# Optimization experiments

Measured on AMD Instinct MI355X. Metric: run time of the kernel, lower is better.

Reference implementation:

```python
import jax, jax.numpy as jnp
import numpy as np

N = 8192          # tokens
CD = 512          # coarse_dim
FD = 512          # fine_dim
CB = 4096         # coarse codebook size
FB = 8192         # fine codebook size
COST = 0.25       # commitment cost
LRELU = 0.1
EPS = 1e-5


def _vq(x, emb):
    # squared-distance cdist: [n, K]
    d = jnp.sum(x * x, axis=1, keepdims=True) + jnp.sum(emb * emb, axis=1) - 2.0 * (x @ emb.T)
    idx = jnp.argmin(d, axis=1)          # temperature=1.0 (updates=0); scaling doesn't change argmin
    q = emb[idx]                          # gather == one-hot @ emb, without materializing one-hot
    e_loss = jnp.mean((jax.lax.stop_gradient(q) - x) ** 2)
    q_loss = jnp.mean((q - jax.lax.stop_gradient(x)) ** 2)
    loss = q_loss + COST * e_loss
    q_st = x + jax.lax.stop_gradient(q - x)   # straight-through
    return q_st, loss


def _mlp(x, w, b, g, be):
    # Linear (torch: x @ W.T + b) -> LayerNorm -> LeakyReLU(0.1)
    h = x @ w.T + b
    m = jnp.mean(h, axis=-1, keepdims=True)
    v = jnp.var(h, axis=-1, keepdims=True)
    h = (h - m) / jnp.sqrt(v + EPS) * g + be
    return jnp.where(h > 0, h, LRELU * h)


def setup_inputs() -> dict:
    key = jax.random.key(0)
    ks = jax.random.split(key, 6)
    xav_c = float(np.sqrt(6.0 / (CB + CD)))
    xav_f = float(np.sqrt(6.0 / (FB + FD)))
    lin_s = float(np.sqrt(1.0 / CD))
    return {
        'z': jax.random.normal(ks[0], (N, CD + FD), dtype=jnp.float32),
        'coarse_emb': jax.random.uniform(ks[1], (CB, CD), jnp.float32, -xav_c, xav_c),
        'fine_emb': jax.random.uniform(ks[2], (FB, FD), jnp.float32, -xav_f, xav_f),
        'w_c2f': jax.random.uniform(ks[3], (FD, CD), jnp.float32, -lin_s, lin_s),
        'b_c2f': jnp.zeros((FD,), jnp.float32),
        'g_c2f': jnp.ones((FD,), jnp.float32),
        'be_c2f': jnp.zeros((FD,), jnp.float32),
        'w_f2c': jax.random.uniform(ks[4], (CD, FD), jnp.float32, -lin_s, lin_s),
        'b_f2c': jnp.zeros((CD,), jnp.float32),
        'g_f2c': jnp.ones((CD,), jnp.float32),
        'be_f2c': jnp.zeros((CD,), jnp.float32),
        'gate_c_raw': jnp.float32(0.5),
        'gate_f_raw': jnp.float32(0.5),
    }


def reference(z, coarse_emb, fine_emb, w_c2f, b_c2f, g_c2f, be_c2f,
              w_f2c, b_f2c, g_f2c, be_f2c, gate_c_raw, gate_f_raw):
    split = z.shape[1] // 2
    z_coarse, z_fine = z[:, :split], z[:, split:]

    z_coarse_q, coarse_loss = _vq(z_coarse, coarse_emb)
    coarse_influence = _mlp(jax.lax.stop_gradient(z_coarse_q), w_c2f, b_c2f, g_c2f, be_c2f)
    gate_c = jax.nn.sigmoid(gate_c_raw)

    residual = z_fine - gate_c * coarse_influence
    z_fine_q, fine_loss = _vq(residual, fine_emb)

    fine_feedback = _mlp(jax.lax.stop_gradient(z_fine_q), w_f2c, b_f2c, g_f2c, be_f2c)
    gate_f = jax.nn.sigmoid(gate_f_raw)

    z_coarse_corrected = z_coarse_q + 0.1 * gate_f * fine_feedback
    z_fine_reconstructed = z_fine_q + gate_c * coarse_influence
    z_hierarchical = jnp.concatenate([z_coarse_corrected, z_fine_reconstructed], axis=1)
    vq_loss = coarse_loss + fine_loss
    return z_hierarchical, vq_loss
```

## Files before the change

kernel.cpp:

```cpp
#include <hip/hip_runtime.h>
#include <hip/hip_bf16.h>
#include <cstdint>
#include <cstddef>

#define KD 512

#define OFF_CN   0u
#define OFF_FN   16384u
#define OFF_ZN   49152u
#define OFF_RN   81920u
#define OFF_LOSS 114688u
#define OFF_AMC  114944u
#define OFF_AMF  180480u
#define OFF_CEH  246016u
#define OFF_CEL  4440320u
#define OFF_FEH  8634624u
#define OFF_FEL  17023232u
#define OFF_ZCH  25411840u
#define OFF_ZCL  33800448u
#define OFF_RH   42189056u
#define OFF_RL   50577664u
#define OFF_W1H  58966272u
#define OFF_W1L  59490560u
#define OFF_W2H  60014848u
#define OFF_W2L  60539136u
#define OFF_H    61063424u
#define OFF_INFL 77840640u


typedef __attribute__((ext_vector_type(8))) short bf16x8;
typedef __attribute__((ext_vector_type(4))) float f32x4;

__device__ __forceinline__ bf16x8 as_bf16x8(int4 v) {
  union { int4 i; bf16x8 b; } u; u.i = v; return u.b;
}

__device__ __forceinline__ float block_sum(float v, float* sred) {
#pragma unroll
  for (int off = 32; off > 0; off >>= 1) v += __shfl_down(v, off, 64);
  if ((threadIdx.x & 63) == 0) sred[threadIdx.x >> 6] = v;
  __syncthreads();
  float r = sred[0] + sred[1] + sred[2] + sred[3];
  __syncthreads();
  return r;
}

__device__ __forceinline__ float sigmoidf_(float x) { return 1.0f / (1.0f + expf(-x)); }

__device__ __forceinline__ void split_bf16(float v, __hip_bfloat16* hi, __hip_bfloat16* lo) {
  __hip_bfloat16 h = __float2bfloat16(v);
  *hi = h;
  *lo = __float2bfloat16(v - __bfloat162float(h));
}

__global__ __launch_bounds__(256) void prep(
    const float* __restrict__ ce, const float* __restrict__ fe, const float* __restrict__ z,
    const float* __restrict__ w1, const float* __restrict__ w2,
    float* __restrict__ cn, float* __restrict__ fn, float* __restrict__ zn,
    __hip_bfloat16* __restrict__ ceH, __hip_bfloat16* __restrict__ ceL,
    __hip_bfloat16* __restrict__ feH, __hip_bfloat16* __restrict__ feL,
    __hip_bfloat16* __restrict__ zcH, __hip_bfloat16* __restrict__ zcL,
    __hip_bfloat16* __restrict__ w1H, __hip_bfloat16* __restrict__ w1L,
    __hip_bfloat16* __restrict__ w2H, __hip_bfloat16* __restrict__ w2L,
    float* __restrict__ lossp) {
  __shared__ float sred[4];
  const int b = blockIdx.x, t = threadIdx.x;
  const float* src;
  float* nd = nullptr;
  __hip_bfloat16 *dh, *dl;
  int fragMode = 0;
  size_t row;
  if (b < 4096) {
    row = b; src = ce + row * KD; nd = cn + row; dh = ceH; dl = ceL; fragMode = 1;
  } else if (b < 12288) {
    row = b - 4096; src = fe + row * KD; nd = fn + row; dh = feH; dl = feL; fragMode = 1;
  } else if (b < 20480) {
    row = b - 12288; src = z + row * 1024; nd = zn + row; dh = zcH; dl = zcL;
  } else if (b < 20992) {
    row = b - 20480; src = w1 + row * KD; dh = w1H; dl = w1L;
  } else {
    row = b - 20992; src = w2 + row * KD; dh = w2H; dl = w2L;
  }
  float acc = 0.0f;
  if (fragMode) {
    float v0 = src[t], v1 = src[t + 256];
    acc = v0 * v0 + v1 * v1;
  } else {
#pragma unroll
    for (int j = 0; j < 2; ++j) {
      int c = t + j * 256;
      float v = src[c];
      acc += v * v;
      __hip_bfloat16 h, l;
      split_bf16(v, &h, &l);
      dh[row * KD + c] = h;
      dl[row * KD + c] = l;
    }
  }
  if (nd) {
    float s = block_sum(acc, sred);
    if (t == 0) nd[0] = s;
  } else {
    __syncthreads();
    __syncthreads();
  }
  if (fragMode && t < 64) {
    union { int4 i; __hip_bfloat16 s[8]; } ph, pl;
#pragma unroll
    for (int j = 0; j < 8; ++j) {
      float v = src[8 * t + j];
      split_bf16(v, &ph.s[j], &pl.s[j]);
    }
    const int chunkIdx = (int)(((row >> 4) * 16 + (t >> 2)) * 64 +
                               ((size_t)((t & 3) << 4) | (row & 15)));
    ((int4*)dh)[chunkIdx] = ph.i;
    ((int4*)dl)[chunkIdx] = pl.i;
  }
  if (b == 20480 && t == 0) lossp[0] = 0.0f;
}

__global__ __launch_bounds__(256) void vq6(
    const int4* __restrict__ AfH, const int4* __restrict__ AfL,
    const __hip_bfloat16* __restrict__ Bh, const __hip_bfloat16* __restrict__ Bl,
    const float* __restrict__ qn, const float* __restrict__ cn,
    unsigned long long* __restrict__ amin) {
  __shared__ __align__(16) __hip_bfloat16 sBh[2][128 * 32];
  __shared__ __align__(16) __hip_bfloat16 sBl[2][128 * 32];
  const int t = threadIdx.x;
  const int w = t >> 6, l = t & 63;
  const int rowTile = blockIdx.y << 7;
  const int colTile = blockIdx.x << 7;
  const int wr = (w >> 1) << 6;
  const int wc = (w & 1) << 6;

  const int srow = t >> 2;
  const int sb = t & 3;
  const int skE = sb << 3;
  const int swz = (sb ^ ((srow >> 1) & 3)) << 3;
  const int wOff0 = (srow << 5) + swz;
  const int wOff1 = ((srow + 64) << 5) + swz;
  const size_t br0 = (size_t)(colTile + srow) * KD;
  const size_t br1 = (size_t)(colTile + 64 + srow) * KD;

  const int fr = l & 15;
  const int q = l >> 4;

  int aB[4];
#pragma unroll
  for (int mt = 0; mt < 4; ++mt)
    aB[mt] = (((rowTile + wr + (mt << 4)) >> 4) << 10) + l;

  f32x4 acc[4][4];
#pragma unroll
  for (int i = 0; i < 4; ++i)
#pragma unroll
    for (int j = 0; j < 4; ++j) acc[i][j] = (f32x4){0.f, 0.f, 0.f, 0.f};

  int4 rBh0 = *(const int4*)(Bh + br0 + skE);
  int4 rBh1 = *(const int4*)(Bh + br1 + skE);
  int4 rBl0 = *(const int4*)(Bl + br0 + skE);
  int4 rBl1 = *(const int4*)(Bl + br1 + skE);
  int4 aH[4], aL[4];
#pragma unroll
  for (int mt = 0; mt < 4; ++mt) {
    aH[mt] = AfH[aB[mt]];
    aL[mt] = AfL[aB[mt]];
  }

  int p = 0;
  for (int kk = 0; kk < KD; kk += 32) {
    *(int4*)(sBh[p] + wOff0) = rBh0; *(int4*)(sBh[p] + wOff1) = rBh1;
    *(int4*)(sBl[p] + wOff0) = rBl0; *(int4*)(sBl[p] + wOff1) = rBl1;
    __syncthreads();

    bf16x8 afh[4], afl[4];
#pragma unroll
    for (int mt = 0; mt < 4; ++mt) {
      afh[mt] = as_bf16x8(aH[mt]);
      afl[mt] = as_bf16x8(aL[mt]);
    }

    const int nkc = (kk + 32 < KD) ? ((kk >> 5) + 1) : 0;
    const int nkE = nkc << 5;
    rBh0 = *(const int4*)(Bh + br0 + nkE + skE);
    rBh1 = *(const int4*)(Bh + br1 + nkE + skE);
    rBl0 = *(const int4*)(Bl + br0 + nkE + skE);
    rBl1 = *(const int4*)(Bl + br1 + nkE + skE);
#pragma unroll
    for (int mt = 0; mt < 4; ++mt) {
      aH[mt] = AfH[aB[mt] + (nkc << 6)];
      aL[mt] = AfL[aB[mt] + (nkc << 6)];
    }

    bf16x8 bfh[4], bfl[4];
#pragma unroll
    for (int nt = 0; nt < 4; ++nt) {
      const int rB = wc + (nt << 4) + fr;
      const int o = (rB << 5) + ((q ^ ((rB >> 1) & 3)) << 3);
      bfh[nt] = *(const bf16x8*)(sBh[p] + o);
      bfl[nt] = *(const bf16x8*)(sBl[p] + o);
    }
#pragma unroll
    for (int mt = 0; mt < 4; ++mt)
#pragma unroll
      for (int nt = 0; nt < 4; ++nt) {
        acc[mt][nt] = __builtin_amdgcn_mfma_f32_16x16x32_bf16(afh[mt], bfh[nt], acc[mt][nt], 0, 0, 0);
        acc[mt][nt] = __builtin_amdgcn_mfma_f32_16x16x32_bf16(afh[mt], bfl[nt], acc[mt][nt], 0, 0, 0);
        acc[mt][nt] = __builtin_amdgcn_mfma_f32_16x16x32_bf16(afl[mt], bfh[nt], acc[mt][nt], 0, 0, 0);
      }
    p ^= 1;
  }

#pragma unroll
  for (int nt = 0; nt < 4; ++nt) {
    const int query = colTile + wc + (nt << 4) + fr;
    const float xn = qn[query];
    unsigned long long key = ~0ULL;
#pragma unroll
    for (int mt = 0; mt < 4; ++mt) {
#pragma unroll
      for (int reg = 0; reg < 4; ++reg) {
        const int code = rowTile + wr + (mt << 4) + (q << 2) + reg;
        float d = (xn + cn[code]) - 2.0f * acc[mt][nt][reg];
        unsigned ub = __float_as_uint(d);
        ub = (ub & 0x80000000u) ? ~ub : (ub | 0x80000000u);
        unsigned long long k2 = ((unsigned long long)ub << 32) | (unsigned long long)(unsigned)code;
        if (k2 < key) key = k2;
      }
    }
    unsigned long long o1 = __shfl_xor(key, 16, 64);
    if (o1 < key) key = o1;
    unsigned long long o2 = __shfl_xor(key, 32, 64);
    if (o2 < key) key = o2;
    if (l < 16) atomicMin(amin + colTile + wc + (nt << 4) + l, key);
  }
}

__global__ __launch_bounds__(256) void mlp6(
    const int4* __restrict__ AfH, const int4* __restrict__ AfL,
    const unsigned long long* __restrict__ gather,
    const __hip_bfloat16* __restrict__ Bh, const __hip_bfloat16* __restrict__ Bl,
    const float* __restrict__ bias, float* __restrict__ C) {
  __shared__ __align__(16) __hip_bfloat16 sAh[128 * 32];
  __shared__ __align__(16) __hip_bfloat16 sAl[128 * 32];
  __shared__ __align__(16) __hip_bfloat16 sBh[128 * 32];
  __shared__ __align__(16) __hip_bfloat16 sBl[128 * 32];
  const int t = threadIdx.x;
  const int w = t >> 6, l = t & 63;
  const int rowTile = blockIdx.y << 7;
  const int colTile = blockIdx.x << 7;
  const int wr = (w >> 1) << 6;
  const int wc = (w & 1) << 6;

  const int srow = t >> 2;
  const int sb = t & 3;
  const int skE = sb << 3;
  const int swz = (sb ^ ((srow >> 1) & 3)) << 3;
  const int wOff0 = (srow << 5) + swz;
  const int wOff1 = ((srow + 64) << 5) + swz;

  unsigned i0 = ((const unsigned*)gather)[2 * (rowTile + srow)];
  unsigned i1 = ((const unsigned*)gather)[2 * (rowTile + 64 + srow)];
  const int a0 = (int)((i0 >> 4) << 10) + (sb << 4) + (int)(i0 & 15);
  const int a1 = (int)((i1 >> 4) << 10) + (sb << 4) + (int)(i1 & 15);
  const size_t br0 = (size_t)(colTile + srow) * KD;
  const size_t br1 = (size_t)(colTile + 64 + srow) * KD;

  const int fr = l & 15;
  const int q = l >> 4;
  const int foff = (q ^ ((fr >> 1) & 3)) << 3;

  f32x4 acc[4][4];
#pragma unroll
  for (int i = 0; i < 4; ++i)
#pragma unroll
    for (int j = 0; j < 4; ++j) acc[i][j] = (f32x4){0.f, 0.f, 0.f, 0.f};

  for (int kk = 0; kk < KD; kk += 32) {
    const int kc64 = (kk >> 5) << 6;
    int4 vAh0 = AfH[a0 + kc64];
    int4 vAh1 = AfH[a1 + kc64];
    int4 vAl0 = AfL[a0 + kc64];
    int4 vAl1 = AfL[a1 + kc64];
    int4 vBh0 = *(const int4*)(Bh + br0 + kk + skE);
    int4 vBh1 = *(const int4*)(Bh + br1 + kk + skE);
    int4 vBl0 = *(const int4*)(Bl + br0 + kk + skE);
    int4 vBl1 = *(const int4*)(Bl + br1 + kk + skE);
    __syncthreads();
    *(int4*)(sAh + wOff0) = vAh0; *(int4*)(sAh + wOff1) = vAh1;
    *(int4*)(sAl + wOff0) = vAl0; *(int4*)(sAl + wOff1) = vAl1;
    *(int4*)(sBh + wOff0) = vBh0; *(int4*)(sBh + wOff1) = vBh1;
    *(int4*)(sBl + wOff0) = vBl0; *(int4*)(sBl + wOff1) = vBl1;
    __syncthreads();

    bf16x8 afh[4], afl[4], bfh[4], bfl[4];
#pragma unroll
    for (int mt = 0; mt < 4; ++mt) {
      const int rA = wr + (mt << 4) + fr;
      const int o = (rA << 5) + ((q ^ ((rA >> 1) & 3)) << 3);
      afh[mt] = *(const bf16x8*)(sAh + o);
      afl[mt] = *(const bf16x8*)(sAl + o);
    }
#pragma unroll
    for (int nt = 0; nt < 4; ++nt) {
      const int rB = wc + (nt << 4) + fr;
      const int o = (rB << 5) + ((q ^ ((rB >> 1) & 3)) << 3);
      bfh[nt] = *(const bf16x8*)(sBh + o);
      bfl[nt] = *(const bf16x8*)(sBl + o);
    }
#pragma unroll
    for (int mt = 0; mt < 4; ++mt)
#pragma unroll
      for (int nt = 0; nt < 4; ++nt) {
        acc[mt][nt] = __builtin_amdgcn_mfma_f32_16x16x32_bf16(afh[mt], bfh[nt], acc[mt][nt], 0, 0, 0);
        acc[mt][nt] = __builtin_amdgcn_mfma_f32_16x16x32_bf16(afh[mt], bfl[nt], acc[mt][nt], 0, 0, 0);
        acc[mt][nt] = __builtin_amdgcn_mfma_f32_16x16x32_bf16(afl[mt], bfh[nt], acc[mt][nt], 0, 0, 0);
      }
  }

  const int quad = l >> 4;
#pragma unroll
  for (int mt = 0; mt < 4; ++mt) {
#pragma unroll
    for (int reg = 0; reg < 4; ++reg) {
      const int row = rowTile + wr + (mt << 4) + (quad << 2) + reg;
#pragma unroll
      for (int nt = 0; nt < 4; ++nt) {
        const int col = colTile + wc + (nt << 4) + fr;
        C[(size_t)row * KD + col] = acc[mt][nt][reg] + bias[col];
      }
    }
  }
}

__global__ __launch_bounds__(256) void ln_residual(
    const float* __restrict__ h, const float* __restrict__ g, const float* __restrict__ be,
    const float* __restrict__ z, const float* __restrict__ gRaw,
    __hip_bfloat16* __restrict__ infl, float* __restrict__ rn,
    __hip_bfloat16* __restrict__ rH, __hip_bfloat16* __restrict__ rL) {
  __shared__ float sred[4];
  const int row = blockIdx.x, t = threadIdx.x;
  const size_t base = (size_t)row * KD;
  float h0 = h[base + t], h1 = h[base + t + 256];
  float m = block_sum(h0 + h1, sred) * (1.0f / 512.0f);
  float d0 = h0 - m, d1 = h1 - m;
  float var = block_sum(d0 * d0 + d1 * d1, sred) * (1.0f / 512.0f);
  float sq = sqrtf(var + 1e-5f);
  float gc = sigmoidf_(gRaw[0]);
  float v0 = d0 / sq * g[t] + be[t];
  float v1 = d1 / sq * g[t + 256] + be[t + 256];
  v0 = v0 > 0.0f ? v0 : 0.1f * v0;
  v1 = v1 > 0.0f ? v1 : 0.1f * v1;
  infl[base + t] = __float2bfloat16(v0);
  infl[base + t + 256] = __float2bfloat16(v1);
  float zf0 = z[(size_t)row * 1024 + 512 + t];
  float zf1 = z[(size_t)row * 1024 + 512 + t + 256];
  float r0 = zf0 - gc * v0, r1 = zf1 - gc * v1;
  __hip_bfloat16 hh, ll;
  split_bf16(r0, &hh, &ll);
  rH[base + t] = hh; rL[base + t] = ll;
  split_bf16(r1, &hh, &ll);
  rH[base + t + 256] = hh; rL[base + t + 256] = ll;
  float rs = block_sum(r0 * r0 + r1 * r1, sred);
  if (t == 0) rn[row] = rs;
}

__global__ __launch_bounds__(256) void finalize(
    const float* __restrict__ h, const float* __restrict__ g, const float* __restrict__ be,
    const __hip_bfloat16* __restrict__ infl,
    const unsigned long long* __restrict__ amc, const unsigned long long* __restrict__ amf,
    const float* __restrict__ z, const float* __restrict__ ce, const float* __restrict__ fe,
    const float* __restrict__ gcRaw, const float* __restrict__ gfRaw,
    float* __restrict__ out, float* __restrict__ lossp) {
  __shared__ float sred[4];
  const int row = blockIdx.x, t = threadIdx.x;
  const size_t base = (size_t)row * KD;
  float h0 = h[base + t], h1 = h[base + t + 256];
  float m = block_sum(h0 + h1, sred) * (1.0f / 512.0f);
  float d0 = h0 - m, d1 = h1 - m;
  float var = block_sum(d0 * d0 + d1 * d1, sred) * (1.0f / 512.0f);
  float sq = sqrtf(var + 1e-5f);
  float fb0 = d0 / sq * g[t] + be[t];
  float fb1 = d1 / sq * g[t + 256] + be[t + 256];
  fb0 = fb0 > 0.0f ? fb0 : 0.1f * fb0;
  fb1 = fb1 > 0.0f ? fb1 : 0.1f * fb1;
  float gc = sigmoidf_(gcRaw[0]);
  float gf = sigmoidf_(gfRaw[0]);
  unsigned ic = (unsigned)(amc[row] & 0xffffffffULL);
  unsigned ifx = (unsigned)(amf[row] & 0xffffffffULL);
  float loc = 0.0f;
#pragma unroll
  for (int j = 0; j < 2; ++j) {
    int c = t + j * 256;
    float fb = j ? fb1 : fb0;
    float qc = ce[(size_t)ic * KD + c];
    float qf = fe[(size_t)ifx * KD + c];
    float zc = z[(size_t)row * 1024 + c];
    float zf = z[(size_t)row * 1024 + 512 + c];
    float fl = __bfloat162float(infl[base + c]);
    out[(size_t)row * 1024 + c] = qc + 0.1f * gf * fb;
    out[(size_t)row * 1024 + 512 + c] = qf + gc * fl;
    float dc = qc - zc;
    float res = zf - gc * fl;
    float df = qf - res;
    loc += dc * dc + df * df;
  }
  float ls = block_sum(loc, sred);
  if (t == 0) atomicAdd(lossp, ls);
}

__global__ void loss_write(const float* __restrict__ lossp, float* __restrict__ out) {
  out[0] = 1.25f * lossp[0] / (8192.0f * 512.0f);
}

extern "C" void kernel_launch(void* const* d_in, const int* in_sizes, int n_in,
                              void* d_out, int out_size, void* d_ws, size_t ws_size,
                              hipStream_t stream) {
  const float* z      = (const float*)d_in[0];
  const float* ce     = (const float*)d_in[1];
  const float* fe     = (const float*)d_in[2];
  const float* w_c2f  = (const float*)d_in[3];
  const float* b_c2f  = (const float*)d_in[4];
  const float* g_c2f  = (const float*)d_in[5];
  const float* be_c2f = (const float*)d_in[6];
  const float* w_f2c  = (const float*)d_in[7];
  const float* b_f2c  = (const float*)d_in[8];
  const float* g_f2c  = (const float*)d_in[9];
  const float* be_f2c = (const float*)d_in[10];
  const float* gcRaw  = (const float*)d_in[11];
  const float* gfRaw  = (const float*)d_in[12];
  float* out = (float*)d_out;
  char* ws = (char*)d_ws;

  float* cn = (float*)(ws + OFF_CN);
  float* fn = (float*)(ws + OFF_FN);
  float* zn = (float*)(ws + OFF_ZN);
  float* rn = (float*)(ws + OFF_RN);
  float* lossp = (float*)(ws + OFF_LOSS);
  unsigned long long* amc = (unsigned long long*)(ws + OFF_AMC);
  unsigned long long* amf = (unsigned long long*)(ws + OFF_AMF);
  __hip_bfloat16* ceH = (__hip_bfloat16*)(ws + OFF_CEH);
  __hip_bfloat16* ceL = (__hip_bfloat16*)(ws + OFF_CEL);
  __hip_bfloat16* feH = (__hip_bfloat16*)(ws + OFF_FEH);
  __hip_bfloat16* feL = (__hip_bfloat16*)(ws + OFF_FEL);
  __hip_bfloat16* zcH = (__hip_bfloat16*)(ws + OFF_ZCH);
  __hip_bfloat16* zcL = (__hip_bfloat16*)(ws + OFF_ZCL);
  __hip_bfloat16* rH  = (__hip_bfloat16*)(ws + OFF_RH);
  __hip_bfloat16* rL  = (__hip_bfloat16*)(ws + OFF_RL);
  __hip_bfloat16* w1H = (__hip_bfloat16*)(ws + OFF_W1H);
  __hip_bfloat16* w1L = (__hip_bfloat16*)(ws + OFF_W1L);
  __hip_bfloat16* w2H = (__hip_bfloat16*)(ws + OFF_W2H);
  __hip_bfloat16* w2L = (__hip_bfloat16*)(ws + OFF_W2L);
  float* h = (float*)(ws + OFF_H);
  __hip_bfloat16* infl = (__hip_bfloat16*)(ws + OFF_INFL);

  hipMemsetAsync(ws + OFF_AMC, 0xFF, 131072, stream);

  prep<<<21504, 256, 0, stream>>>(ce, fe, z, w_c2f, w_f2c, cn, fn, zn,
                                  ceH, ceL, feH, feL, zcH, zcL,
                                  w1H, w1L, w2H, w2L, lossp);

  vq6<<<dim3(64, 32), 256, 0, stream>>>((const int4*)ceH, (const int4*)ceL,
                                        zcH, zcL, zn, cn, amc);

  mlp6<<<dim3(4, 64), 256, 0, stream>>>((const int4*)ceH, (const int4*)ceL, amc,
                                        w1H, w1L, b_c2f, h);

  ln_residual<<<8192, 256, 0, stream>>>(h, g_c2f, be_c2f, z, gcRaw, infl, rn, rH, rL);

  vq6<<<dim3(64, 64), 256, 0, stream>>>((const int4*)feH, (const int4*)feL,
                                        rH, rL, rn, fn, amf);

  mlp6<<<dim3(4, 64), 256, 0, stream>>>((const int4*)feH, (const int4*)feL, amf,
                                        w2H, w2L, b_f2c, h);

  finalize<<<8192, 256, 0, stream>>>(h, g_f2c, be_f2c, infl, amc, amf, z, ce, fe,
                                     gcRaw, gfRaw, out, lossp);
  loss_write<<<1, 1, 0, stream>>>(lossp, out + (size_t)8192 * 1024);
}
```

Baseline: 640.8 us.

## Stage VQ codebook tiles via direct global-to-LDS loads with triple buffering

The VQ distance GEMM kernel now copies B tiles straight from global memory into LDS with global_load_lds, instead of going through registers and explicit LDS stores. It uses a three-deep LDS ring with prefetch two steps ahead, one barrier per k-step, and a fully unrolled k loop. The XOR swizzle moves from the LDS write address to the global source address. The aim is to free VGPRs and LDS-store issue slots and to hide load latency better, with s_setprio raised around the MFMA block. The cost is more LDS use and reliance on implicit vmcnt waits to order the DMA writes before the reads.

Measured after the change: 622.3 us. 2.9% less time.

```diff
diff --git a/kernel.cpp b/kernel.cpp
--- a/kernel.cpp
+++ b/kernel.cpp
@@ -33,6 +33,12 @@
 
 __device__ __forceinline__ bf16x8 as_bf16x8(int4 v) {
   union { int4 i; bf16x8 b; } u; u.i = v; return u.b;
+}
+
+__device__ __forceinline__ void gl_lds16(const void* g, void* l) {
+  __builtin_amdgcn_global_load_lds(
+      (const __attribute__((address_space(1))) void*)g,
+      (__attribute__((address_space(3))) void*)l, 16, 0, 0);
 }
 
 __device__ __forceinline__ float block_sum(float v, float* sred) {
@@ -119,13 +125,13 @@
   if (b == 20480 && t == 0) lossp[0] = 0.0f;
 }
 
-__global__ __launch_bounds__(256) void vq6(
+__global__ __launch_bounds__(256) void vq7(
     const int4* __restrict__ AfH, const int4* __restrict__ AfL,
     const __hip_bfloat16* __restrict__ Bh, const __hip_bfloat16* __restrict__ Bl,
     const float* __restrict__ qn, const float* __restrict__ cn,
     unsigned long long* __restrict__ amin) {
-  __shared__ __align__(16) __hip_bfloat16 sBh[2][128 * 32];
-  __shared__ __align__(16) __hip_bfloat16 sBl[2][128 * 32];
+  __shared__ __align__(16) __hip_bfloat16 sBh[3][128 * 32];
+  __shared__ __align__(16) __hip_bfloat16 sBl[3][128 * 32];
   const int t = threadIdx.x;
   const int w = t >> 6, l = t & 63;
   const int rowTile = blockIdx.y << 7;
@@ -133,14 +139,12 @@
   const int wr = (w >> 1) << 6;
   const int wc = (w & 1) << 6;
 
-  const int srow = t >> 2;
-  const int sb = t & 3;
-  const int skE = sb << 3;
-  const int swz = (sb ^ ((srow >> 1) & 3)) << 3;
-  const int wOff0 = (srow << 5) + swz;
-  const int wOff1 = ((srow + 64) << 5) + swz;
-  const size_t br0 = (size_t)(colTile + srow) * KD;
-  const size_t br1 = (size_t)(colTile + 64 + srow) * KD;
+  const int rl = l >> 2;
+  const int sbp = (l & 3) ^ ((l >> 3) & 3);
+  const size_t gOff0 = (size_t)(colTile + (w << 5) + rl) * KD + (sbp << 3);
+  const size_t gOff1 = gOff0 + (size_t)16 * KD;
+  const int lOff0 = (w << 5) << 5;
+  const int lOff1 = lOff0 + (16 << 5);
 
   const int fr = l & 15;
   const int q = l >> 4;
@@ -156,22 +160,27 @@
 #pragma unroll
     for (int j = 0; j < 4; ++j) acc[i][j] = (f32x4){0.f, 0.f, 0.f, 0.f};
 
-  int4 rBh0 = *(const int4*)(Bh + br0 + skE);
-  int4 rBh1 = *(const int4*)(Bh + br1 + skE);
-  int4 rBl0 = *(const int4*)(Bl + br0 + skE);
-  int4 rBl1 = *(const int4*)(Bl + br1 + skE);
+#define STAGE_B(bi, ck) do {                                      \
+    gl_lds16(Bh + gOff0 + ((size_t)(ck) << 5), &sBh[bi][lOff0]);  \
+    gl_lds16(Bh + gOff1 + ((size_t)(ck) << 5), &sBh[bi][lOff1]);  \
+    gl_lds16(Bl + gOff0 + ((size_t)(ck) << 5), &sBl[bi][lOff0]);  \
+    gl_lds16(Bl + gOff1 + ((size_t)(ck) << 5), &sBl[bi][lOff1]);  \
+  } while (0)
+
   int4 aH[4], aL[4];
-#pragma unroll
-  for (int mt = 0; mt < 4; ++mt) {
-    aH[mt] = AfH[aB[mt]];
-    aL[mt] = AfL[aB[mt]];
-  }
-
-  int p = 0;
-  for (int kk = 0; kk < KD; kk += 32) {
-    *(int4*)(sBh[p] + wOff0) = rBh0; *(int4*)(sBh[p] + wOff1) = rBh1;
-    *(int4*)(sBl[p] + wOff0) = rBl0; *(int4*)(sBl[p] + wOff1) = rBl1;
-    __syncthreads();
+  STAGE_B(0, 0);
+  STAGE_B(1, 1);
+#pragma unroll
+  for (int mt = 0; mt < 4; ++mt) { aH[mt] = AfH[aB[mt]]; aL[mt] = AfL[aB[mt]]; }
+  __builtin_amdgcn_sched_barrier(0);
+  asm volatile("s_waitcnt vmcnt(0)" ::: "memory");
+
+#pragma unroll
+  for (int i = 0; i < 16; ++i) {
+    __builtin_amdgcn_s_barrier();
+    __builtin_amdgcn_sched_barrier(0);
+    if (i + 2 < 16) STAGE_B((i + 2) % 3, i + 2);
+    __builtin_amdgcn_sched_barrier(0);
 
     bf16x8 afh[4], afl[4];
 #pragma unroll
@@ -179,26 +188,24 @@
       afh[mt] = as_bf16x8(aH[mt]);
       afl[mt] = as_bf16x8(aL[mt]);
     }
-
-    const int nkc = (kk + 32 < KD) ? ((kk >> 5) + 1) : 0;
-    const int nkE = nkc << 5;
-    rBh0 = *(const int4*)(Bh + br0 + nkE + skE);
-    rBh1 = *(const int4*)(Bh + br1 + nkE + skE);
-    rBl0 = *(const int4*)(Bl + br0 + nkE + skE);
-    rBl1 = *(const int4*)(Bl + br1 + nkE + skE);
-#pragma unroll
-    for (int mt = 0; mt < 4; ++mt) {
-      aH[mt] = AfH[aB[mt] + (nkc << 6)];
-      aL[mt] = AfL[aB[mt] + (nkc << 6)];
-    }
-
+    if (i + 1 < 16) {
+#pragma unroll
+      for (int mt = 0; mt < 4; ++mt) {
+        aH[mt] = AfH[aB[mt] + ((i + 1) << 6)];
+        aL[mt] = AfL[aB[mt] + ((i + 1) << 6)];
+      }
+    }
+    __builtin_amdgcn_sched_barrier(0);
+
+    __builtin_amdgcn_s_setprio(1);
+    const int cb = i % 3;
     bf16x8 bfh[4], bfl[4];
 #pragma unroll
     for (int nt = 0; nt < 4; ++nt) {
       const int rB = wc + (nt << 4) + fr;
       const int o = (rB << 5) + ((q ^ ((rB >> 1) & 3)) << 3);
-      bfh[nt] = *(const bf16x8*)(sBh[p] + o);
-      bfl[nt] = *(const bf16x8*)(sBl[p] + o);
+      bfh[nt] = *(const bf16x8*)(sBh[cb] + o);
+      bfl[nt] = *(const bf16x8*)(sBl[cb] + o);
     }
 #pragma unroll
     for (int mt = 0; mt < 4; ++mt)
@@ -208,7 +215,7 @@
         acc[mt][nt] = __builtin_amdgcn_mfma_f32_16x16x32_bf16(afh[mt], bfl[nt], acc[mt][nt], 0, 0, 0);
         acc[mt][nt] = __builtin_amdgcn_mfma_f32_16x16x32_bf16(afl[mt], bfh[nt], acc[mt][nt], 0, 0, 0);
       }
-    p ^= 1;
+    __builtin_amdgcn_s_setprio(0);
   }
 
 #pragma unroll
@@ -268,7 +275,6 @@
 
   const int fr = l & 15;
   const int q = l >> 4;
-  const int foff = (q ^ ((fr >> 1) & 3)) << 3;
 
   f32x4 acc[4][4];
 #pragma unroll
@@ -460,7 +466,7 @@
                                   ceH, ceL, feH, feL, zcH, zcL,
                                   w1H, w1L, w2H, w2L, lossp);
 
-  vq6<<<dim3(64, 32), 256, 0, stream>>>((const int4*)ceH, (const int4*)ceL,
+  vq7<<<dim3(64, 32), 256, 0, stream>>>((const int4*)ceH, (const int4*)ceL,
                                         zcH, zcL, zn, cn, amc);
 
   mlp6<<<dim3(4, 64), 256, 0, stream>>>((const int4*)ceH, (const int4*)ceL, amc,
@@ -468,7 +474,7 @@
 
   ln_residual<<<8192, 256, 0, stream>>>(h, g_c2f, be_c2f, z, gcRaw, infl, rn, rH, rL);
 
-  vq6<<<dim3(64, 64), 256, 0, stream>>>((const int4*)feH, (const int4*)feL,
+  vq7<<<dim3(64, 64), 256, 0, stream>>>((const int4*)feH, (const int4*)feL,
                                         rH, rL, rn, fn, amf);
 
   mlp6<<<dim3(4, 64), 256, 0, stream>>>((const int4*)feH, (const int4*)feL, amf,
```
